# Optimization experiments

Measured on AMD Instinct MI355X. Metric: run time of the kernel, lower is better.

## Reference

```python
import jax, jax.numpy as jnp
import numpy as np

B, T, M, P = 128, 65, 512, 512  # batch, T, encoder_hidden, decoder_hidden


def setup_inputs() -> dict:
    key = jax.random.key(0)
    ks = jax.random.split(key, 10)
    Tm1 = T - 1
    f32 = jnp.float32

    def init(k, shape, scale=0.02):
        return jax.random.normal(k, shape, f32) * scale

    return {
        "X_encoded": jax.random.normal(ks[0], (B, Tm1, M), f32),
        "y_prev": jax.random.normal(ks[1], (B, Tm1), f32),
        # attn_layer: Linear(2P+M -> M), Tanh, Linear(M -> 1)
        "W_a1": init(ks[2], (M, 2 * P + M)), "b_a1": jnp.zeros((M,), f32),
        "W_a2": init(ks[3], (1, M)), "b_a2": jnp.zeros((1,), f32),
        # LSTM(input_size=1, hidden=P); gate order i,f,g,o
        "W_ih": init(ks[4], (4 * P, 1)), "W_hh": init(ks[5], (4 * P, P)),
        "b_ih": jnp.zeros((4 * P,), f32), "b_hh": jnp.zeros((4 * P,), f32),
        # fc: Linear(M+1 -> 1); original code sets fc.weight ~ N(0,1)
        "W_fc": jax.random.normal(ks[6], (1, M + 1), f32), "b_fc": jnp.zeros((1,), f32),
        # fc_final: Linear(P+M -> 1)
        "W_fin": init(ks[7], (1, P + M)), "b_fin": jnp.zeros((1,), f32),
    }


def reference(X_encoded, y_prev, W_a1, b_a1, W_a2, b_a2,
              W_ih, W_hh, b_ih, b_hh, W_fc, b_fc, W_fin, b_fin):
    Bq, Tm1, Mm = X_encoded.shape
    Pp = W_hh.shape[1]
    dt = X_encoded.dtype

    def step(carry, y_t):
        d, c, _ = carry  # (B,P), (B,P)
        dd = jnp.broadcast_to(d[:, None, :], (Bq, Tm1, Pp))
        cc = jnp.broadcast_to(c[:, None, :], (Bq, Tm1, Pp))
        x = jnp.concatenate([dd, cc, X_encoded], axis=2)  # (B,Tm1,2P+M)
        h = jnp.tanh(jnp.einsum('btf,ef->bte', x, W_a1) + b_a1)
        e = jnp.einsum('bte,oe->bto', h, W_a2) + b_a2  # (B,Tm1,1)
        # Faithful to the original buggy torch views: raw row-major reshape
        # (B,Tm1)->(Tm1,B), softmax over dim=1, reshape back (NOT a transpose).
        beta = jax.nn.softmax(e.reshape(Tm1, Bq), axis=1).reshape(Bq, Tm1)
        context = jnp.einsum('bt,btm->bm', beta, X_encoded)  # (B,M)
        y_tilde = jnp.concatenate([context, y_t[:, None]], axis=1) @ W_fc.T + b_fc  # (B,1)
        gates = y_tilde @ W_ih.T + b_ih + d @ W_hh.T + b_hh  # (B,4P)
        i, f, g, o = jnp.split(gates, 4, axis=1)
        c_new = jax.nn.sigmoid(f) * c + jax.nn.sigmoid(i) * jnp.tanh(g)
        d_new = jax.nn.sigmoid(o) * jnp.tanh(c_new)
        return (d_new, c_new, context), None

    init = (jnp.zeros((Bq, Pp), dt), jnp.zeros((Bq, Pp), dt), jnp.zeros((Bq, Mm), dt))
    (d, c, context), _ = jax.lax.scan(step, init, y_prev.T)  # scan over Tm1 steps
    return jnp.concatenate([d, context], axis=1) @ W_fin.T + b_fin  # (B,1)
```

## Files before the change

kernel.cpp:

```cpp
#include <hip/hip_runtime.h>
#include <hip/hip_cooperative_groups.h>

namespace cg = cooperative_groups;

typedef _Float16 v8h __attribute__((ext_vector_type(8)));
typedef _Float16 h2v __attribute__((ext_vector_type(2)));
typedef float v4f __attribute__((ext_vector_type(4)));

#define SCOPE_AGENT __HIP_MEMORY_SCOPE_AGENT

static __device__ __forceinline__ uint32_t ald32(const uint32_t* p) {
    return __hip_atomic_load(p, __ATOMIC_RELAXED, SCOPE_AGENT);
}
static __device__ __forceinline__ uint64_t ald64(const uint64_t* p) {
    return __hip_atomic_load(p, __ATOMIC_RELAXED, SCOPE_AGENT);
}
static __device__ __forceinline__ void ast32(uint32_t* p, uint32_t v) {
    __hip_atomic_store(p, v, __ATOMIC_RELAXED, SCOPE_AGENT);
}
static __device__ __forceinline__ v8h mkv8(uint64_t lo, uint64_t hi) {
    union { uint64_t q[2]; v8h h; } u; u.q[0] = lo; u.q[1] = hi; return u.h;
}
static __device__ __forceinline__ uint32_t packh(float a, float b) {
    uint16_t ua = __builtin_bit_cast(uint16_t, (_Float16)a);
    uint16_t ub = __builtin_bit_cast(uint16_t, (_Float16)b);
    return (uint32_t)ua | ((uint32_t)ub << 16);
}
static __device__ __forceinline__ float fast_rcp(float x) {
    float y;
    asm("v_rcp_f32 %0, %1" : "=v"(y) : "v"(x));
    return y;
}
static __device__ __forceinline__ float fast_tanh(float x) {
    float e = __expf(2.0f * x);
    return 1.0f - 2.0f * fast_rcp(e + 1.0f);
}
static __device__ __forceinline__ float fast_sigmoid(float x) {
    return fast_rcp(1.0f + __expf(-x));
}
static __device__ __forceinline__ v8h cvt8(const float* p) {
    float4 a = *(const float4*)p;
    float4 b = *(const float4*)(p + 4);
    v8h h;
    h[0] = (_Float16)a.x; h[1] = (_Float16)a.y; h[2] = (_Float16)a.z; h[3] = (_Float16)a.w;
    h[4] = (_Float16)b.x; h[5] = (_Float16)b.y; h[6] = (_Float16)b.z; h[7] = (_Float16)b.w;
    return h;
}

#define FWA_OFF 32768
#define FWB_OFF 65536

static __device__ __forceinline__ void wait_lines(const uint32_t* base, int n, uint32_t target) {
    if ((int)threadIdx.x < n) {
        const uint32_t* p = base + threadIdx.x * 32;
        while (ald32(p) < target) __builtin_amdgcn_s_sleep(1);
    }
    __syncthreads();
    asm volatile("" ::: "memory");
}
static __device__ __forceinline__ void publish_lines(uint32_t* base, int n, int stride_u32, uint32_t v) {
    asm volatile("s_waitcnt vmcnt(0)" ::: "memory");
    __syncthreads();
    if ((int)threadIdx.x < n) ast32(base + threadIdx.x * stride_u32, v);
}

__global__ __launch_bounds__(512, 2) void fused_decoder(
    const float* __restrict__ Xe, const float* __restrict__ ypr,
    const float* __restrict__ Wa1, const float* __restrict__ ba1,
    const float* __restrict__ Wa2, const float* __restrict__ ba2,
    const float* __restrict__ Wih, const float* __restrict__ Whh,
    const float* __restrict__ bih, const float* __restrict__ bhh,
    const float* __restrict__ Wfc, const float* __restrict__ bfc,
    const float* __restrict__ Wfin, const float* __restrict__ bfin,
    float* __restrict__ out,
    uint32_t* __restrict__ ctrs,
    _Float16* __restrict__ Ab,
    float* __restrict__ glin,
    float* __restrict__ partS,
    _Float16* __restrict__ hx,
    _Float16* __restrict__ Wa1a,
    _Float16* __restrict__ Whh16)
{
    cg::grid_group gg = cg::this_grid();
    const int bid = blockIdx.x;
    const int tid = threadIdx.x;
    const int wave = tid >> 6, lane = tid & 63;
    const int l15 = lane & 15, kq = lane >> 4;
    const int gt = bid * 512 + tid;

    __shared__ __align__(16) char arena[143888];

    gg.sync();

    if (gt < 8192) {
        int row = gt >> 4, seg = gt & 15;
        const float* src = Wa1 + (size_t)row * 1536 + seg * 64;
        _Float16* dp = Wa1a + (size_t)row * 1024 + seg * 64;
#pragma unroll
        for (int i = 0; i < 8; ++i) *(v8h*)(dp + i * 8) = cvt8(src + i * 8);
    } else if (gt < 24576) {
        int u = gt - 8192;
        int row = u >> 3, seg = u & 7;
        const float* src = Whh + (size_t)row * 512 + seg * 64;
        _Float16* dp = Whh16 + (size_t)row * 512 + seg * 64;
#pragma unroll
        for (int i = 0; i < 8; ++i) *(v8h*)(dp + i * 8) = cvt8(src + i * 8);
    } else if (gt < 26624) {
        uint64_t* p = (uint64_t*)Ab + (size_t)(gt - 24576) * 16;
#pragma unroll
        for (int i = 0; i < 16; ++i) p[i] = 0ull;
    } else if (gt < 124928) {
        ctrs[gt - 26624] = 0u;
    }
    {
        const int wg = bid * 8 + wave;
        const int mt = wg >> 2;
        const int nq = wg & 3;
        const float* Abase = Xe + (size_t)(mt * 16 + l15) * 512 + kq * 8;
        v8h afr[16];
#pragma unroll
        for (int ks = 0; ks < 16; ++ks) afr[ks] = cvt8(Abase + ks * 32);
#pragma unroll
        for (int i = 0; i < 8; ++i) {
            const int nt = nq * 8 + i;
            const float* Bbase = Wa1 + (size_t)(nt * 16 + l15) * 1536 + 1024 + kq * 8;
            v4f acc = {};
#pragma unroll 4
            for (int ks = 0; ks < 16; ++ks)
                acc = __builtin_amdgcn_mfma_f32_16x16x32_f16(afr[ks], cvt8(Bbase + ks * 32), acc, 0, 0, 0);
            const float bav = ba1[nt * 16 + l15];
            _Float16* hrow = hx + (size_t)(mt * 16 + kq * 4) * 512 + nt * 16 + l15;
#pragma unroll
            for (int r = 0; r < 4; ++r) hrow[(size_t)r * 512] = (_Float16)(acc[r] + bav);
        }
    }
    gg.sync();

    if (bid >= 128 && bid < 192) return;

    if (bid < 128) {
        const int r = bid >> 4, w = bid & 15;
        const int g16 = r * 16;
        const uint32_t* fPbase = ctrs + (size_t)(r * 128 + w * 8) * 32;
        uint32_t* fWAbase = ctrs + FWA_OFF + (size_t)(r * 128 + w) * 32;
        uint32_t* fWBbase = ctrs + FWB_OFF + (size_t)(r * 128 + w) * 32;
        _Float16* hxL = (_Float16*)arena;
        float* red = (float*)(arena + 65536);
        float* s_tile = (float*)(arena + 131072);
        float* w2l = (float*)(arena + 133120);

        for (int cmb = tid; cmb < 1024; cmb += 512) {
            const int b = cmb >> 6, tt = cmb & 63;
            const _Float16* src = hx + ((size_t)(g16 + b) * 64 + tt) * 512 + w * 32;
#pragma unroll
            for (int c = 0; c < 4; ++c)
                *(v8h*)(hxL + ((size_t)(c * 1024 + cmb) << 3)) = *(const v8h*)(src + c * 8);
        }
        if (tid < 32) w2l[tid] = Wa2[w * 32 + tid];
        __syncthreads();

        const uint64_t* abase = (const uint64_t*)Ab + (size_t)(g16 + l15) * 256 + kq * 2;
        v8h B0r[4], B1r[4];
#pragma unroll
        for (int k2 = 0; k2 < 4; ++k2) {
            const int kk = wave * 4 + k2;
            B0r[k2] = *(const v8h*)(Wa1a + (size_t)(w * 32 + l15) * 1024 + kk * 32 + kq * 8);
            B1r[k2] = *(const v8h*)(Wa1a + (size_t)(w * 32 + 16 + l15) * 1024 + kk * 32 + kq * 8);
        }
        v8h Bgr[8][2];
#pragma unroll
        for (int nt = 0; nt < 8; ++nt)
#pragma unroll
            for (int i = 0; i < 2; ++i)
                Bgr[nt][i] = *(const v8h*)(Whh16 + (size_t)(w * 128 + nt * 16 + l15) * 512
                                           + (wave * 2 + i) * 32 + kq * 8);
        float bbv[4];
#pragma unroll
        for (int j = 0; j < 4; ++j) {
            const int gcol = w * 128 + ((tid + j * 512) & 127);
            bbv[j] = bih[gcol] + bhh[gcol];
        }
        uint32_t* partOut = (uint32_t*)partS;

        for (int t = 0; t < 64; ++t) {
            if (t) wait_lines(fPbase, 8, (uint32_t)t);
            uint64_t ls[8], lg[4];
#pragma unroll
            for (int k2 = 0; k2 < 4; ++k2) {
                ls[2 * k2]     = ald64(abase + (wave * 4 + k2) * 8);
                ls[2 * k2 + 1] = ald64(abase + (wave * 4 + k2) * 8 + 1);
            }
#pragma unroll
            for (int i = 0; i < 2; ++i) {
                lg[2 * i]     = ald64(abase + (wave * 2 + i) * 8);
                lg[2 * i + 1] = ald64(abase + (wave * 2 + i) * 8 + 1);
            }
            v4f a0 = {}, a1 = {};
#pragma unroll
            for (int k2 = 0; k2 < 4; ++k2) {
                const v8h af = mkv8(ls[2 * k2], ls[2 * k2 + 1]);
                a0 = __builtin_amdgcn_mfma_f32_16x16x32_f16(af, B0r[k2], a0, 0, 0, 0);
                a1 = __builtin_amdgcn_mfma_f32_16x16x32_f16(af, B1r[k2], a1, 0, 0, 0);
            }
#pragma unroll
            for (int rr = 0; rr < 4; ++rr) {
                red[wave * 512 + (kq * 4 + rr) * 32 + l15] = a0[rr];
                red[wave * 512 + (kq * 4 + rr) * 32 + 16 + l15] = a1[rr];
            }
            __syncthreads();
            {
                float ssum = 0.0f;
#pragma unroll
                for (int wv = 0; wv < 8; ++wv) ssum += red[wv * 512 + tid];
                s_tile[tid] = ssum;
            }
            __syncthreads();

#pragma unroll
            for (int cc = 0; cc < 2; ++cc) {
                const int cmb = tid + cc * 512;
                const int b = cmb >> 6, tt = cmb & 63;
                const _Float16* hb = hxL + ((size_t)cmb << 3);
                float acc = 0.0f;
#pragma unroll
                for (int q = 0; q < 4; ++q) {
                    const v8h hv = *(const v8h*)(hb + ((size_t)q << 13));
#pragma unroll
                    for (int j = 0; j < 8; ++j)
                        acc += w2l[q * 8 + j] *
                               fast_tanh(s_tile[b * 32 + q * 8 + j] + (float)hv[j]);
                }
                const int pg = r * 8 + (b >> 1);
                ast32(partOut + (((size_t)pg * 16 + w) * 2 + (b & 1)) * 64 + tt,
                      __builtin_bit_cast(uint32_t, acc));
            }
            publish_lines(fWAbase, 8, 16 * 32, (uint32_t)(t + 1));

#pragma unroll
            for (int nt = 0; nt < 8; ++nt) {
                v4f ag = {};
#pragma unroll
                for (int i = 0; i < 2; ++i)
                    ag = __builtin_amdgcn_mfma_f32_16x16x32_f16(
                        mkv8(lg[2 * i], lg[2 * i + 1]), Bgr[nt][i], ag, 0, 0, 0);
#pragma unroll
                for (int rr = 0; rr < 4; ++rr)
                    red[wave * 2048 + (kq * 4 + rr) * 128 + nt * 16 + l15] = ag[rr];
            }
            __syncthreads();
#pragma unroll
            for (int j = 0; j < 4; ++j) {
                const int o = tid + j * 512;
                float gsum = 0.0f;
#pragma unroll
                for (int wv = 0; wv < 8; ++wv) gsum += red[wv * 2048 + o];
                ast32((uint32_t*)glin + (size_t)(g16 + (o >> 7)) * 2048 + w * 128 + (o & 127),
                      __builtin_bit_cast(uint32_t, gsum + bbv[j]));
            }
            publish_lines(fWBbase, 8, 16 * 32, (uint32_t)(t + 1));
        }
    } else {
        const int p = bid - 192, b0 = 2 * p, r = p >> 3, pl = p & 7;
        uint32_t* fPbase = ctrs + (size_t)(r * 128 + pl) * 32;
        const uint32_t* fWAbase = ctrs + FWA_OFF + (size_t)(r * 128 + pl * 16) * 32;
        const uint32_t* fWBbase = ctrs + FWB_OFF + (size_t)(r * 128 + pl * 16) * 32;
        _Float16* XeL = (_Float16*)arena;
        float* sc = (float*)(arena + 131072);
        float* dstL = (float*)(arena + 131584);
        float* ctxl = (float*)(arena + 135680);
        float* ytl = (float*)(arena + 139776);
        float* red0 = (float*)(arena + 139784);

        {
            const float* xsrc = Xe + (size_t)b0 * 64 * 512;
#pragma unroll
            for (int i = 0; i < 16; ++i) {
                const int u = tid + i * 512;
                *(v8h*)(XeL + (size_t)u * 8) = cvt8(xsrc + (size_t)u * 8);
            }
        }
        const float wih_i = Wih[tid], wih_f = Wih[512 + tid],
                    wih_g = Wih[1024 + tid], wih_o = Wih[1536 + tid];
        float creg[2] = {0.0f, 0.0f}, dreg[2] = {0.0f, 0.0f};
        uint32_t* Abu = (uint32_t*)Ab;
        const uint32_t* partB = (const uint32_t*)partS;
        __syncthreads();

        for (int t = 0; t < 64; ++t) {
            wait_lines(fWAbase, 16, (uint32_t)(t + 1));
            {
                const int cmb = tid >> 2, wq = tid & 3;
                const int blv = cmb >> 6, tt = cmb & 63;
                float acc = 0.0f;
#pragma unroll
                for (int i = 0; i < 4; ++i)
                    acc += __builtin_bit_cast(float,
                        ald32(partB + (((size_t)p * 16 + wq * 4 + i) * 2 + blv) * 64 + tt));
                acc += __shfl_xor(acc, 1, 64);
                acc += __shfl_xor(acc, 2, 64);
                if (wq == 0) sc[cmb] = acc;
            }
            __syncthreads();

            if (tid < 64) {
                float m2 = fmaxf(sc[tid], sc[tid + 64]);
#pragma unroll
                for (int off = 32; off; off >>= 1) m2 = fmaxf(m2, __shfl_xor(m2, off, 64));
                float e0v = __expf(sc[tid] - m2);
                float e1v = __expf(sc[tid + 64] - m2);
                sc[tid] = e0v; sc[tid + 64] = e1v;
                float ssum = e0v + e1v;
#pragma unroll
                for (int off = 32; off; off >>= 1) ssum += __shfl_xor(ssum, off, 64);
                if (tid == 0) red0[0] = 1.0f / ssum;
            }
            __syncthreads();
            const float inv = red0[0];

            wait_lines(fWBbase, 16, (uint32_t)(t + 1));
            uint32_t gv[2][4];
#pragma unroll
            for (int blv = 0; blv < 2; ++blv) {
                const uint32_t* gb = (const uint32_t*)glin + (size_t)(b0 + blv) * 2048 + tid;
                gv[blv][0] = ald32(gb);
                gv[blv][1] = ald32(gb + 512);
                gv[blv][2] = ald32(gb + 1024);
                gv[blv][3] = ald32(gb + 1536);
            }

            {
                const int blv = tid >> 8, m2 = (tid & 255) * 2;
                const _Float16* xb = XeL + (size_t)blv * 64 * 512 + m2;
                float a0 = 0.0f, a1 = 0.0f;
#pragma unroll 8
                for (int tt = 0; tt < 64; ++tt) {
                    const h2v xv = *(const h2v*)(xb + (size_t)tt * 512);
                    const float bta = sc[blv * 64 + tt];
                    a0 += bta * (float)xv[0];
                    a1 += bta * (float)xv[1];
                }
                ctxl[blv * 512 + m2] = a0 * inv;
                ctxl[blv * 512 + m2 + 1] = a1 * inv;
            }
            __syncthreads();

            if (tid < 128) {
                const int blv = tid >> 6, l2 = tid & 63;
                float acc = 0.0f;
#pragma unroll
                for (int j = 0; j < 8; ++j) acc += ctxl[blv * 512 + l2 * 8 + j] * Wfc[l2 * 8 + j];
#pragma unroll
                for (int off = 32; off; off >>= 1) acc += __shfl_xor(acc, off, 64);
                if (l2 == 0)
                    ytl[blv] = acc + Wfc[512] * ypr[(size_t)(b0 + blv) * 64 + t] + bfc[0];
            }
            __syncthreads();

#pragma unroll
            for (int blv = 0; blv < 2; ++blv) {
                const float yt = ytl[blv];
                float ii = __builtin_bit_cast(float, gv[blv][0]) + yt * wih_i;
                float ff = __builtin_bit_cast(float, gv[blv][1]) + yt * wih_f;
                float ggv = __builtin_bit_cast(float, gv[blv][2]) + yt * wih_g;
                float oo = __builtin_bit_cast(float, gv[blv][3]) + yt * wih_o;
                float cn = fast_sigmoid(ff) * creg[blv] + fast_sigmoid(ii) * fast_tanh(ggv);
                float dn = fast_sigmoid(oo) * fast_tanh(cn);
                creg[blv] = cn;
                dreg[blv] = dn;
                float dp = __shfl_xor(dn, 1, 64);
                float cp = __shfl_xor(cn, 1, 64);
                if (!(tid & 1)) {
                    ast32(Abu + (size_t)(b0 + blv) * 512 + (tid >> 1), packh(dn, dp));
                    ast32(Abu + (size_t)(b0 + blv) * 512 + 256 + (tid >> 1), packh(cn, cp));
                }
            }
            if (t == 63) {
                dstL[tid] = dreg[0];
                dstL[512 + tid] = dreg[1];
                __syncthreads();
                if (tid < 128) {
                    const int blv = tid >> 6, l2 = tid & 63;
                    float acc = 0.0f;
#pragma unroll
                    for (int j = 0; j < 8; ++j) {
                        const int e = l2 * 8 + j;
                        acc += dstL[blv * 512 + e] * Wfin[e] + ctxl[blv * 512 + e] * Wfin[512 + e];
                    }
#pragma unroll
                    for (int off = 32; off; off >>= 1) acc += __shfl_xor(acc, off, 64);
                    if (l2 == 0) out[b0 + blv] = acc + bfin[0];
                }
            }
            publish_lines(fPbase, 16, 8 * 32, (uint32_t)(t + 1));
        }
    }
}

extern "C" void kernel_launch(void* const* d_in, const int* in_sizes, int n_in,
                              void* d_out, int out_size, void* d_ws, size_t ws_size,
                              hipStream_t stream)
{
    const float* Xe   = (const float*)d_in[0];
    const float* ypr  = (const float*)d_in[1];
    const float* Wa1  = (const float*)d_in[2];
    const float* ba1  = (const float*)d_in[3];
    const float* Wa2  = (const float*)d_in[4];
    const float* ba2  = (const float*)d_in[5];
    const float* Wih  = (const float*)d_in[6];
    const float* Whh  = (const float*)d_in[7];
    const float* bih  = (const float*)d_in[8];
    const float* bhh  = (const float*)d_in[9];
    const float* Wfc  = (const float*)d_in[10];
    const float* bfc  = (const float*)d_in[11];
    const float* Wfin = (const float*)d_in[12];
    const float* bfin = (const float*)d_in[13];
    float* out = (float*)d_out;

    char* w = (char*)d_ws;
    uint32_t* ctrs  = (uint32_t*)w;                 w += 393216;
    _Float16* Ab    = (_Float16*)w;                 w += (size_t)128 * 1024 * 2;
    float*    glin  = (float*)w;                    w += (size_t)128 * 2048 * 4;
    float*    partS = (float*)w;                    w += (size_t)64 * 16 * 2 * 64 * 4;
    _Float16* hx    = (_Float16*)w;                 w += (size_t)8192 * 512 * 2;
    _Float16* Wa1a  = (_Float16*)w;                 w += (size_t)512 * 1024 * 2;
    _Float16* Whh16 = (_Float16*)w;                 w += (size_t)2048 * 512 * 2;

    void* args[] = {
        (void*)&Xe, (void*)&ypr, (void*)&Wa1, (void*)&ba1, (void*)&Wa2, (void*)&ba2,
        (void*)&Wih, (void*)&Whh, (void*)&bih, (void*)&bhh, (void*)&Wfc, (void*)&bfc,
        (void*)&Wfin, (void*)&bfin, (void*)&out,
        (void*)&ctrs, (void*)&Ab, (void*)&glin, (void*)&partS, (void*)&hx,
        (void*)&Wa1a, (void*)&Whh16
    };
    hipLaunchCooperativeKernel((const void*)fused_decoder, dim3(256), dim3(512),
                               args, 0, stream);
}
```

Before: 906.1 us.

## Replace counter flags with sentinel-value polling on double-buffered state and partial sums

Drops the per-step counter publish/wait handshakes (the fP and fWA flag lines) between attention blocks and LSTM blocks. Consumers now poll the data itself until no sentinel NaN pattern remains, then reset the slot to the sentinel. The Ab state buffer and the partS partial-sum buffer are double-buffered by step parity, and partS is re-laid out so each consumer reads contiguous 64-bit words. This removes the flag round-trip latency and extra syncthreads on each step. In exchange it relies on relaxed atomic ordering, and a real value that happens to equal the sentinel bit pattern would stall or mis-synchronise.

```diff
diff --git a/kernel.cpp b/kernel.cpp
--- a/kernel.cpp
+++ b/kernel.cpp
@@ -9,6 +9,11 @@
 
 #define SCOPE_AGENT __HIP_MEMORY_SCOPE_AGENT
 
+#define SA32 0x7E007E00u
+#define SA64 0x7E007E007E007E00ull
+#define SP32 0x7FC0DEADu
+#define SP64 0x7FC0DEAD7FC0DEADull
+
 static __device__ __forceinline__ uint32_t ald32(const uint32_t* p) {
     return __hip_atomic_load(p, __ATOMIC_RELAXED, SCOPE_AGENT);
 }
@@ -16,6 +21,9 @@
     return __hip_atomic_load(p, __ATOMIC_RELAXED, SCOPE_AGENT);
 }
 static __device__ __forceinline__ void ast32(uint32_t* p, uint32_t v) {
+    __hip_atomic_store(p, v, __ATOMIC_RELAXED, SCOPE_AGENT);
+}
+static __device__ __forceinline__ void ast64(uint64_t* p, uint64_t v) {
     __hip_atomic_store(p, v, __ATOMIC_RELAXED, SCOPE_AGENT);
 }
 static __device__ __forceinline__ v8h mkv8(uint64_t lo, uint64_t hi) {
@@ -47,7 +55,6 @@
     return h;
 }
 
-#define FWA_OFF 32768
 #define FWB_OFF 65536
 
 static __device__ __forceinline__ void wait_lines(const uint32_t* base, int n, uint32_t target) {
@@ -109,8 +116,16 @@
         uint64_t* p = (uint64_t*)Ab + (size_t)(gt - 24576) * 16;
 #pragma unroll
         for (int i = 0; i < 16; ++i) p[i] = 0ull;
-    } else if (gt < 124928) {
-        ctrs[gt - 26624] = 0u;
+    } else if (gt < 28672) {
+        uint64_t* p = (uint64_t*)Ab + 32768 + (size_t)(gt - 26624) * 16;
+#pragma unroll
+        for (int i = 0; i < 16; ++i) p[i] = SA64;
+    } else if (gt < 36864) {
+        uint64_t* p = (uint64_t*)partS + (size_t)(gt - 28672) * 16;
+#pragma unroll
+        for (int i = 0; i < 16; ++i) p[i] = SP64;
+    } else if (gt < 69632) {
+        ctrs[FWB_OFF + (gt - 36864)] = 0u;
     }
     {
         const int wg = bid * 8 + wave;
@@ -141,8 +156,6 @@
     if (bid < 128) {
         const int r = bid >> 4, w = bid & 15;
         const int g16 = r * 16;
-        const uint32_t* fPbase = ctrs + (size_t)(r * 128 + w * 8) * 32;
-        uint32_t* fWAbase = ctrs + FWA_OFF + (size_t)(r * 128 + w) * 32;
         uint32_t* fWBbase = ctrs + FWB_OFF + (size_t)(r * 128 + w) * 32;
         _Float16* hxL = (_Float16*)arena;
         float* red = (float*)(arena + 65536);
@@ -159,7 +172,7 @@
         if (tid < 32) w2l[tid] = Wa2[w * 32 + tid];
         __syncthreads();
 
-        const uint64_t* abase = (const uint64_t*)Ab + (size_t)(g16 + l15) * 256 + kq * 2;
+        const uint64_t* Abq = (const uint64_t*)Ab;
         v8h B0r[4], B1r[4];
 #pragma unroll
         for (int k2 = 0; k2 < 4; ++k2) {
@@ -183,18 +196,32 @@
         uint32_t* partOut = (uint32_t*)partS;
 
         for (int t = 0; t < 64; ++t) {
-            if (t) wait_lines(fPbase, 8, (uint32_t)t);
+            const uint64_t* ab = Abq + (size_t)(t & 1) * 32768
+                               + (size_t)(g16 + l15) * 256 + kq * 2;
             uint64_t ls[8], lg[4];
-#pragma unroll
-            for (int k2 = 0; k2 < 4; ++k2) {
-                ls[2 * k2]     = ald64(abase + (wave * 4 + k2) * 8);
-                ls[2 * k2 + 1] = ald64(abase + (wave * 4 + k2) * 8 + 1);
-            }
-#pragma unroll
-            for (int i = 0; i < 2; ++i) {
-                lg[2 * i]     = ald64(abase + (wave * 2 + i) * 8);
-                lg[2 * i + 1] = ald64(abase + (wave * 2 + i) * 8 + 1);
-            }
+            for (;;) {
+                bool ok = true;
+#pragma unroll
+                for (int k2 = 0; k2 < 4; ++k2) {
+                    ls[2 * k2]     = ald64(ab + (wave * 4 + k2) * 8);
+                    ls[2 * k2 + 1] = ald64(ab + (wave * 4 + k2) * 8 + 1);
+                }
+#pragma unroll
+                for (int i = 0; i < 2; ++i) {
+                    lg[2 * i]     = ald64(ab + (wave * 2 + i) * 8);
+                    lg[2 * i + 1] = ald64(ab + (wave * 2 + i) * 8 + 1);
+                }
+#pragma unroll
+                for (int j = 0; j < 8; ++j)
+                    ok = ok && ((uint32_t)ls[j] != SA32) && ((uint32_t)(ls[j] >> 32) != SA32);
+#pragma unroll
+                for (int j = 0; j < 4; ++j)
+                    ok = ok && ((uint32_t)lg[j] != SA32) && ((uint32_t)(lg[j] >> 32) != SA32);
+                if (ok) break;
+                __builtin_amdgcn_s_sleep(0);
+            }
+            asm volatile("" ::: "memory");
+
             v4f a0 = {}, a1 = {};
 #pragma unroll
             for (int k2 = 0; k2 < 4; ++k2) {
@@ -231,10 +258,10 @@
                                fast_tanh(s_tile[b * 32 + q * 8 + j] + (float)hv[j]);
                 }
                 const int pg = r * 8 + (b >> 1);
-                ast32(partOut + (((size_t)pg * 16 + w) * 2 + (b & 1)) * 64 + tt,
+                ast32(partOut + (size_t)(t & 1) * 131072
+                      + (((size_t)pg * 2 + (b & 1)) * 64 + tt) * 16 + w,
                       __builtin_bit_cast(uint32_t, acc));
             }
-            publish_lines(fWAbase, 8, 16 * 32, (uint32_t)(t + 1));
 
 #pragma unroll
             for (int nt = 0; nt < 8; ++nt) {
@@ -261,8 +288,6 @@
         }
     } else {
         const int p = bid - 192, b0 = 2 * p, r = p >> 3, pl = p & 7;
-        uint32_t* fPbase = ctrs + (size_t)(r * 128 + pl) * 32;
-        const uint32_t* fWAbase = ctrs + FWA_OFF + (size_t)(r * 128 + pl * 16) * 32;
         const uint32_t* fWBbase = ctrs + FWB_OFF + (size_t)(r * 128 + pl * 16) * 32;
         _Float16* XeL = (_Float16*)arena;
         float* sc = (float*)(arena + 131072);
@@ -283,23 +308,35 @@
                     wih_g = Wih[1024 + tid], wih_o = Wih[1536 + tid];
         float creg[2] = {0.0f, 0.0f}, dreg[2] = {0.0f, 0.0f};
         uint32_t* Abu = (uint32_t*)Ab;
-        const uint32_t* partB = (const uint32_t*)partS;
         __syncthreads();
 
+        const int cmbG = tid >> 2, wq = tid & 3;
+        const int blvG = cmbG >> 6, ttG = cmbG & 63;
+
         for (int t = 0; t < 64; ++t) {
-            wait_lines(fWAbase, 16, (uint32_t)(t + 1));
-            {
-                const int cmb = tid >> 2, wq = tid & 3;
-                const int blv = cmb >> 6, tt = cmb & 63;
-                float acc = 0.0f;
-#pragma unroll
-                for (int i = 0; i < 4; ++i)
-                    acc += __builtin_bit_cast(float,
-                        ald32(partB + (((size_t)p * 16 + wq * 4 + i) * 2 + blv) * 64 + tt));
-                acc += __shfl_xor(acc, 1, 64);
-                acc += __shfl_xor(acc, 2, 64);
-                if (wq == 0) sc[cmb] = acc;
-            }
+            uint64_t* gb = (uint64_t*)partS + (size_t)(t & 1) * 65536
+                         + (((size_t)p * 2 + blvG) * 64 + ttG) * 8 + wq * 2;
+            uint64_t q0, q1;
+            for (;;) {
+                q0 = ald64(gb);
+                q1 = ald64(gb + 1);
+                bool ok = ((uint32_t)q0 != SP32) && ((uint32_t)(q0 >> 32) != SP32)
+                       && ((uint32_t)q1 != SP32) && ((uint32_t)(q1 >> 32) != SP32);
+                if (ok) break;
+                __builtin_amdgcn_s_sleep(0);
+            }
+            asm volatile("" ::: "memory");
+            float acc = __builtin_bit_cast(float, (uint32_t)q0)
+                      + __builtin_bit_cast(float, (uint32_t)(q0 >> 32))
+                      + __builtin_bit_cast(float, (uint32_t)q1)
+                      + __builtin_bit_cast(float, (uint32_t)(q1 >> 32));
+            ast64(gb, SP64);
+            ast64(gb + 1, SP64);
+            ast32(Abu + (size_t)(t & 1) * 65536 + (size_t)b0 * 512 + tid, SA32);
+            ast32(Abu + (size_t)(t & 1) * 65536 + (size_t)(b0 + 1) * 512 + tid, SA32);
+            acc += __shfl_xor(acc, 1, 64);
+            acc += __shfl_xor(acc, 2, 64);
+            if (wq == 0) sc[cmbG] = acc;
             __syncthreads();
 
             if (tid < 64) {
@@ -321,11 +358,11 @@
             uint32_t gv[2][4];
 #pragma unroll
             for (int blv = 0; blv < 2; ++blv) {
-                const uint32_t* gb = (const uint32_t*)glin + (size_t)(b0 + blv) * 2048 + tid;
-                gv[blv][0] = ald32(gb);
-                gv[blv][1] = ald32(gb + 512);
-                gv[blv][2] = ald32(gb + 1024);
-                gv[blv][3] = ald32(gb + 1536);
+                const uint32_t* gb2 = (const uint32_t*)glin + (size_t)(b0 + blv) * 2048 + tid;
+                gv[blv][0] = ald32(gb2);
+                gv[blv][1] = ald32(gb2 + 512);
+                gv[blv][2] = ald32(gb2 + 1024);
+                gv[blv][3] = ald32(gb2 + 1536);
             }
 
             {
@@ -346,16 +383,18 @@
 
             if (tid < 128) {
                 const int blv = tid >> 6, l2 = tid & 63;
-                float acc = 0.0f;
-#pragma unroll
-                for (int j = 0; j < 8; ++j) acc += ctxl[blv * 512 + l2 * 8 + j] * Wfc[l2 * 8 + j];
-#pragma unroll
-                for (int off = 32; off; off >>= 1) acc += __shfl_xor(acc, off, 64);
+                float acc2 = 0.0f;
+#pragma unroll
+                for (int j = 0; j < 8; ++j) acc2 += ctxl[blv * 512 + l2 * 8 + j] * Wfc[l2 * 8 + j];
+#pragma unroll
+                for (int off = 32; off; off >>= 1) acc2 += __shfl_xor(acc2, off, 64);
                 if (l2 == 0)
-                    ytl[blv] = acc + Wfc[512] * ypr[(size_t)(b0 + blv) * 64 + t] + bfc[0];
-            }
-            __syncthreads();
-
+                    ytl[blv] = acc2 + Wfc[512] * ypr[(size_t)(b0 + blv) * 64 + t] + bfc[0];
+            }
+            asm volatile("s_waitcnt vmcnt(0)" ::: "memory");
+            __syncthreads();
+
+            const size_t abOff = (size_t)((t + 1) & 1) * 65536;
 #pragma unroll
             for (int blv = 0; blv < 2; ++blv) {
                 const float yt = ytl[blv];
@@ -370,8 +409,8 @@
                 float dp = __shfl_xor(dn, 1, 64);
                 float cp = __shfl_xor(cn, 1, 64);
                 if (!(tid & 1)) {
-                    ast32(Abu + (size_t)(b0 + blv) * 512 + (tid >> 1), packh(dn, dp));
-                    ast32(Abu + (size_t)(b0 + blv) * 512 + 256 + (tid >> 1), packh(cn, cp));
+                    ast32(Abu + abOff + (size_t)(b0 + blv) * 512 + (tid >> 1), packh(dn, dp));
+                    ast32(Abu + abOff + (size_t)(b0 + blv) * 512 + 256 + (tid >> 1), packh(cn, cp));
                 }
             }
             if (t == 63) {
@@ -380,18 +419,17 @@
                 __syncthreads();
                 if (tid < 128) {
                     const int blv = tid >> 6, l2 = tid & 63;
-                    float acc = 0.0f;
+                    float acc2 = 0.0f;
 #pragma unroll
                     for (int j = 0; j < 8; ++j) {
                         const int e = l2 * 8 + j;
-                        acc += dstL[blv * 512 + e] * Wfin[e] + ctxl[blv * 512 + e] * Wfin[512 + e];
+                        acc2 += dstL[blv * 512 + e] * Wfin[e] + ctxl[blv * 512 + e] * Wfin[512 + e];
                     }
 #pragma unroll
-                    for (int off = 32; off; off >>= 1) acc += __shfl_xor(acc, off, 64);
-                    if (l2 == 0) out[b0 + blv] = acc + bfin[0];
-                }
-            }
-            publish_lines(fPbase, 16, 8 * 32, (uint32_t)(t + 1));
+                    for (int off = 32; off; off >>= 1) acc2 += __shfl_xor(acc2, off, 64);
+                    if (l2 == 0) out[b0 + blv] = acc2 + bfin[0];
+                }
+            }
         }
     }
 }
@@ -418,9 +456,9 @@
 
     char* w = (char*)d_ws;
     uint32_t* ctrs  = (uint32_t*)w;                 w += 393216;
-    _Float16* Ab    = (_Float16*)w;                 w += (size_t)128 * 1024 * 2;
+    _Float16* Ab    = (_Float16*)w;                 w += (size_t)2 * 128 * 1024 * 2;
     float*    glin  = (float*)w;                    w += (size_t)128 * 2048 * 4;
-    float*    partS = (float*)w;                    w += (size_t)64 * 16 * 2 * 64 * 4;
+    float*    partS = (float*)w;                    w += (size_t)2 * 64 * 2 * 64 * 16 * 4;
     _Float16* hx    = (_Float16*)w;                 w += (size_t)8192 * 512 * 2;
     _Float16* Wa1a  = (_Float16*)w;                 w += (size_t)512 * 1024 * 2;
     _Float16* Whh16 = (_Float16*)w;                 w += (size_t)2048 * 512 * 2;
```

Measured after the change: 994.9 us. 9.8% more time.

## Precompute Xe·Wfc projection, defer full context to final step, swizzle LDS reductions

Applied to the files above, without the earlier changes.

Since y_tilde only needs context·Wfc, the kernel precomputes Xe·Wfc per (batch, time) once and forms the per-step value as a beta-weighted dot over 64 scalars. This replaces the per-step 512-wide context accumulation over time, which is now done only at the last step for the final output. The publish of the LSTM state moves ahead of that final-step work, and the LDS reduction buffers get a row-dependent column swizzle to cut bank conflicts. The cost is an extra workspace buffer and a small prologue pass that every thread runs.

```diff
diff --git a/kernel.cpp b/kernel.cpp
--- a/kernel.cpp
+++ b/kernel.cpp
@@ -79,7 +79,8 @@
     float* __restrict__ partS,
     _Float16* __restrict__ hx,
     _Float16* __restrict__ Wa1a,
-    _Float16* __restrict__ Whh16)
+    _Float16* __restrict__ Whh16,
+    float* __restrict__ XW)
 {
     cg::grid_group gg = cg::this_grid();
     const int bid = blockIdx.x;
@@ -111,6 +112,17 @@
         for (int i = 0; i < 16; ++i) p[i] = 0ull;
     } else if (gt < 124928) {
         ctrs[gt - 26624] = 0u;
+    }
+    {
+        const int row = gt >> 4, sub = gt & 15;
+        const float* src = Xe + (size_t)row * 512 + sub * 32;
+        float acc = 0.0f;
+#pragma unroll
+        for (int i = 0; i < 32; ++i)
+            acc += Wfc[sub * 32 + i] * (float)(_Float16)src[i];
+#pragma unroll
+        for (int off = 1; off < 16; off <<= 1) acc += __shfl_xor(acc, off, 64);
+        if (sub == 0) XW[row] = acc;
     }
     {
         const int wg = bid * 8 + wave;
@@ -204,14 +216,17 @@
             }
 #pragma unroll
             for (int rr = 0; rr < 4; ++rr) {
-                red[wave * 512 + (kq * 4 + rr) * 32 + l15] = a0[rr];
-                red[wave * 512 + (kq * 4 + rr) * 32 + 16 + l15] = a1[rr];
+                const int brow = kq * 4 + rr;
+                red[wave * 512 + brow * 32 + ((l15 + 2 * brow) & 31)] = a0[rr];
+                red[wave * 512 + brow * 32 + ((16 + l15 + 2 * brow) & 31)] = a1[rr];
             }
             __syncthreads();
             {
+                const int brow2 = tid >> 5, e2 = tid & 31;
+                const int sidx = brow2 * 32 + ((e2 + 2 * brow2) & 31);
                 float ssum = 0.0f;
 #pragma unroll
-                for (int wv = 0; wv < 8; ++wv) ssum += red[wv * 512 + tid];
+                for (int wv = 0; wv < 8; ++wv) ssum += red[wv * 512 + sidx];
                 s_tile[tid] = ssum;
             }
             __syncthreads();
@@ -244,17 +259,21 @@
                     ag = __builtin_amdgcn_mfma_f32_16x16x32_f16(
                         mkv8(lg[2 * i], lg[2 * i + 1]), Bgr[nt][i], ag, 0, 0, 0);
 #pragma unroll
-                for (int rr = 0; rr < 4; ++rr)
-                    red[wave * 2048 + (kq * 4 + rr) * 128 + nt * 16 + l15] = ag[rr];
+                for (int rr = 0; rr < 4; ++rr) {
+                    const int row = kq * 4 + rr;
+                    red[wave * 2048 + row * 128 + ((nt * 16 + l15 + 2 * row) & 127)] = ag[rr];
+                }
             }
             __syncthreads();
 #pragma unroll
             for (int j = 0; j < 4; ++j) {
                 const int o = tid + j * 512;
+                const int row2 = o >> 7, col2 = o & 127;
+                const int gidx = row2 * 128 + ((col2 + 2 * row2) & 127);
                 float gsum = 0.0f;
 #pragma unroll
-                for (int wv = 0; wv < 8; ++wv) gsum += red[wv * 2048 + o];
-                ast32((uint32_t*)glin + (size_t)(g16 + (o >> 7)) * 2048 + w * 128 + (o & 127),
+                for (int wv = 0; wv < 8; ++wv) gsum += red[wv * 2048 + gidx];
+                ast32((uint32_t*)glin + (size_t)(g16 + row2) * 2048 + w * 128 + col2,
                       __builtin_bit_cast(uint32_t, gsum + bbv[j]));
             }
             publish_lines(fWBbase, 8, 16 * 32, (uint32_t)(t + 1));
@@ -270,6 +289,7 @@
         float* ctxl = (float*)(arena + 135680);
         float* ytl = (float*)(arena + 139776);
         float* red0 = (float*)(arena + 139784);
+        float* XWl = (float*)(arena + 139792);
 
         {
             const float* xsrc = Xe + (size_t)b0 * 64 * 512;
@@ -279,6 +299,7 @@
                 *(v8h*)(XeL + (size_t)u * 8) = cvt8(xsrc + (size_t)u * 8);
             }
         }
+        if (tid < 128) XWl[tid] = XW[(size_t)(b0 + (tid >> 6)) * 64 + (tid & 63)];
         const float wih_i = Wih[tid], wih_f = Wih[512 + tid],
                     wih_g = Wih[1024 + tid], wih_o = Wih[1536 + tid];
         float creg[2] = {0.0f, 0.0f}, dreg[2] = {0.0f, 0.0f};
@@ -321,38 +342,20 @@
             uint32_t gv[2][4];
 #pragma unroll
             for (int blv = 0; blv < 2; ++blv) {
-                const uint32_t* gb = (const uint32_t*)glin + (size_t)(b0 + blv) * 2048 + tid;
-                gv[blv][0] = ald32(gb);
-                gv[blv][1] = ald32(gb + 512);
-                gv[blv][2] = ald32(gb + 1024);
-                gv[blv][3] = ald32(gb + 1536);
-            }
-
-            {
-                const int blv = tid >> 8, m2 = (tid & 255) * 2;
-                const _Float16* xb = XeL + (size_t)blv * 64 * 512 + m2;
-                float a0 = 0.0f, a1 = 0.0f;
-#pragma unroll 8
-                for (int tt = 0; tt < 64; ++tt) {
-                    const h2v xv = *(const h2v*)(xb + (size_t)tt * 512);
-                    const float bta = sc[blv * 64 + tt];
-                    a0 += bta * (float)xv[0];
-                    a1 += bta * (float)xv[1];
-                }
-                ctxl[blv * 512 + m2] = a0 * inv;
-                ctxl[blv * 512 + m2 + 1] = a1 * inv;
-            }
-            __syncthreads();
+                const uint32_t* gb2 = (const uint32_t*)glin + (size_t)(b0 + blv) * 2048 + tid;
+                gv[blv][0] = ald32(gb2);
+                gv[blv][1] = ald32(gb2 + 512);
+                gv[blv][2] = ald32(gb2 + 1024);
+                gv[blv][3] = ald32(gb2 + 1536);
+            }
 
             if (tid < 128) {
                 const int blv = tid >> 6, l2 = tid & 63;
-                float acc = 0.0f;
-#pragma unroll
-                for (int j = 0; j < 8; ++j) acc += ctxl[blv * 512 + l2 * 8 + j] * Wfc[l2 * 8 + j];
-#pragma unroll
-                for (int off = 32; off; off >>= 1) acc += __shfl_xor(acc, off, 64);
+                float v = sc[blv * 64 + l2] * XWl[blv * 64 + l2];
+#pragma unroll
+                for (int off = 32; off; off >>= 1) v += __shfl_xor(v, off, 64);
                 if (l2 == 0)
-                    ytl[blv] = acc + Wfc[512] * ypr[(size_t)(b0 + blv) * 64 + t] + bfc[0];
+                    ytl[blv] = inv * v + Wfc[512] * ypr[(size_t)(b0 + blv) * 64 + t] + bfc[0];
             }
             __syncthreads();
 
@@ -374,24 +377,39 @@
                     ast32(Abu + (size_t)(b0 + blv) * 512 + 256 + (tid >> 1), packh(cn, cp));
                 }
             }
+            publish_lines(fPbase, 16, 8 * 32, (uint32_t)(t + 1));
+
             if (t == 63) {
+                {
+                    const int blv = tid >> 8, m2 = (tid & 255) * 2;
+                    const _Float16* xb = XeL + (size_t)blv * 64 * 512 + m2;
+                    float a0 = 0.0f, a1 = 0.0f;
+#pragma unroll 8
+                    for (int tt = 0; tt < 64; ++tt) {
+                        const h2v xv = *(const h2v*)(xb + (size_t)tt * 512);
+                        const float bta = sc[blv * 64 + tt];
+                        a0 += bta * (float)xv[0];
+                        a1 += bta * (float)xv[1];
+                    }
+                    ctxl[blv * 512 + m2] = a0 * inv;
+                    ctxl[blv * 512 + m2 + 1] = a1 * inv;
+                }
                 dstL[tid] = dreg[0];
                 dstL[512 + tid] = dreg[1];
                 __syncthreads();
                 if (tid < 128) {
                     const int blv = tid >> 6, l2 = tid & 63;
-                    float acc = 0.0f;
+                    float acc2 = 0.0f;
 #pragma unroll
                     for (int j = 0; j < 8; ++j) {
                         const int e = l2 * 8 + j;
-                        acc += dstL[blv * 512 + e] * Wfin[e] + ctxl[blv * 512 + e] * Wfin[512 + e];
+                        acc2 += dstL[blv * 512 + e] * Wfin[e] + ctxl[blv * 512 + e] * Wfin[512 + e];
                     }
 #pragma unroll
-                    for (int off = 32; off; off >>= 1) acc += __shfl_xor(acc, off, 64);
-                    if (l2 == 0) out[b0 + blv] = acc + bfin[0];
+                    for (int off = 32; off; off >>= 1) acc2 += __shfl_xor(acc2, off, 64);
+                    if (l2 == 0) out[b0 + blv] = acc2 + bfin[0];
                 }
             }
-            publish_lines(fPbase, 16, 8 * 32, (uint32_t)(t + 1));
         }
     }
 }
@@ -424,13 +442,14 @@
     _Float16* hx    = (_Float16*)w;                 w += (size_t)8192 * 512 * 2;
     _Float16* Wa1a  = (_Float16*)w;                 w += (size_t)512 * 1024 * 2;
     _Float16* Whh16 = (_Float16*)w;                 w += (size_t)2048 * 512 * 2;
+    float*    XW    = (float*)w;                    w += (size_t)128 * 64 * 4;
 
     void* args[] = {
         (void*)&Xe, (void*)&ypr, (void*)&Wa1, (void*)&ba1, (void*)&Wa2, (void*)&ba2,
         (void*)&Wih, (void*)&Whh, (void*)&bih, (void*)&bhh, (void*)&Wfc, (void*)&bfc,
         (void*)&Wfin, (void*)&bfin, (void*)&out,
         (void*)&ctrs, (void*)&Ab, (void*)&glin, (void*)&partS, (void*)&hx,
-        (void*)&Wa1a, (void*)&Whh16
+        (void*)&Wa1a, (void*)&Whh16, (void*)&XW
     };
     hipLaunchCooperativeKernel((const void*)fused_decoder, dim3(256), dim3(512),
                                args, 0, stream);
```

Measured after the change: 855.5 us. 5.6% less time.
